# Optimization experiments

Measured on AMD Instinct MI355X. Metric: run time of the kernel, lower is better.

## Reference

```python
import jax, jax.numpy as jnp
import numpy as np

DISCOUNT = 0.99
HORIZON = 16


def setup_inputs() -> dict:
    key = jax.random.key(0)
    k1, k2, k3 = jax.random.split(key, 3)
    T, B = 1024, 4096
    rewards = jax.random.normal(k1, (T, B), dtype=jnp.float32)
    values = jax.random.normal(k2, (T, B), dtype=jnp.float32)
    masks = jax.random.uniform(k3, (T, B), dtype=jnp.float32)
    return {"rewards": rewards, "values": values, "masks": masks}


def _n_step_return(rewards, values, masks, gamma, horizon):
    # rewards/values/masks: [T, B]; time_axis == 0
    T = rewards.shape[0]
    rm = rewards * masks  # masked rewards
    # Pad end of time axis with zeros so every window has length `horizon`;
    # out-of-range rewards contribute 0, matching the truncated MC sum.
    pad = jnp.zeros((horizon - 1,) + rm.shape[1:], rm.dtype)
    rm_p = jnp.concatenate([rm, pad], axis=0)  # [T + horizon - 1, B]
    t = jnp.arange(T)
    idx = t[:, None] + jnp.arange(horizon)[None, :]  # [T, horizon]
    windows = rm_p[idx]  # [T, horizon, B]
    disc = jnp.asarray(gamma, rm.dtype) ** jnp.arange(horizon, dtype=rm.dtype)
    g = jnp.einsum('thb,h->tb', windows, disc)  # windowed discounted sums
    # Bootstrap: gamma^{effective_horizon} * V(s_{min(t+horizon-1, T-1)})
    eff_h = (jnp.minimum(t + horizon, T) - t).astype(rm.dtype)  # [T]
    v_idx = jnp.minimum(t + horizon - 1, T - 1)  # [T]
    g = g + (jnp.asarray(gamma, rm.dtype) ** eff_h)[:, None] * values[v_idx]
    return g


def reference(rewards, values, masks):
    return _n_step_return(rewards, values, masks, DISCOUNT, HORIZON)
```

## Files before the change

### kernel.cpp

```cpp
#include <hip/hip_runtime.h>


constexpr int   T_DIM  = 1024;
constexpr int   B_DIM  = 4096;
constexpr int   H      = 16;
constexpr int   CT     = 16;
constexpr int   HALO   = H - 1;
constexpr int   ROWS   = CT + HALO;
constexpr float GAMMA  = 0.99f;

constexpr float gpow_c(int n) {
    float g = 1.0f;
    for (int i = 0; i < n; ++i) g *= GAMMA;
    return g;
}
constexpr float G16 = gpow_c(16);

__global__ __launch_bounds__(256)
void NStepReturn_88691074662796_kernel(const float* __restrict__ rewards,
                                       const float* __restrict__ values,
                                       const float* __restrict__ masks,
                                       float* __restrict__ out)
{
    const int b  = blockIdx.x * 256 + threadIdx.x;
    const int t0 = blockIdx.y * CT;

    float r[ROWS], m[ROWS], v[CT];
    #pragma unroll
    for (int i = 0; i < ROWS; ++i) {
        const int t = t0 + i;
        if (t < T_DIM) {
            r[i] = rewards[t * B_DIM + b];
            m[i] = masks[t * B_DIM + b];
        } else {
            r[i] = 0.0f;
            m[i] = 0.0f;
        }
    }
    #pragma unroll
    for (int i = 0; i < CT; ++i) {
        const int vi = min(t0 + i + H - 1, T_DIM - 1);
        v[i] = values[vi * B_DIM + b];
    }

    #pragma unroll
    for (int i = 0; i < ROWS; ++i) r[i] *= m[i];

    float W = 0.0f;
    #pragma unroll
    for (int h = H - 1; h >= 0; --h) W = r[CT - 1 + h] + GAMMA * W;

    {
        const int t = t0 + CT - 1;
        float gb = G16;
        if (t + H > T_DIM) {
            gb = 1.0f;
            for (int k = 0; k < T_DIM - t; ++k) gb *= GAMMA;
        }
        out[t * B_DIM + b] = W + gb * v[CT - 1];
    }

    #pragma unroll
    for (int j = CT - 2; j >= 0; --j) {
        const int t = t0 + j;
        W = r[j] + GAMMA * W - G16 * r[j + H];

        float gb = G16;
        if (t + H > T_DIM) {
            gb = 1.0f;
            for (int k = 0; k < T_DIM - t; ++k) gb *= GAMMA;
        }
        out[t * B_DIM + b] = W + gb * v[j];
    }
}

extern "C" void kernel_launch(void* const* d_in, const int* in_sizes, int n_in,
                              void* d_out, int out_size, void* d_ws, size_t ws_size,
                              hipStream_t stream) {
    const float* rewards = (const float*)d_in[0];
    const float* values  = (const float*)d_in[1];
    const float* masks   = (const float*)d_in[2];
    float* out = (float*)d_out;

    dim3 grid(B_DIM / 256, T_DIM / CT);
    dim3 block(256);
    NStepReturn_88691074662796_kernel<<<grid, block, 0, stream>>>(rewards, values, masks, out);
}
```

Before: 89.82 us.

## Vectorize n-step return kernel with float4 and shrink time chunk

Each thread now processes four batch columns with float4 loads and stores, which cuts the number of memory instructions. The time chunk shrinks from 16 to 8 rows, and a launch-bounds occupancy hint is added to limit register pressure from the wider per-thread state. The smaller chunk raises the halo re-read overhead (23 rows read per 8 output rows instead of 31 per 16), trading extra memory traffic for more blocks and vector access.

```diff
diff --git a/kernel.cpp b/kernel.cpp
--- a/kernel.cpp
+++ b/kernel.cpp
@@ -3,8 +3,9 @@
 
 constexpr int   T_DIM  = 1024;
 constexpr int   B_DIM  = 4096;
+constexpr int   B4     = B_DIM / 4;
 constexpr int   H      = 16;
-constexpr int   CT     = 16;
+constexpr int   CT     = 8;
 constexpr int   HALO   = H - 1;
 constexpr int   ROWS   = CT + HALO;
 constexpr float GAMMA  = 0.99f;
@@ -16,39 +17,44 @@
 }
 constexpr float G16 = gpow_c(16);
 
-__global__ __launch_bounds__(256)
-void NStepReturn_88691074662796_kernel(const float* __restrict__ rewards,
-                                       const float* __restrict__ values,
-                                       const float* __restrict__ masks,
-                                       float* __restrict__ out)
+__global__ __launch_bounds__(256, 2)
+void NStepReturn_88691074662796_kernel(const float4* __restrict__ rewards,
+                                       const float4* __restrict__ values,
+                                       const float4* __restrict__ masks,
+                                       float4* __restrict__ out)
 {
-    const int b  = blockIdx.x * 256 + threadIdx.x;
+    const int c  = blockIdx.x * 256 + threadIdx.x;
     const int t0 = blockIdx.y * CT;
 
-    float r[ROWS], m[ROWS], v[CT];
+    float4 v[CT];
+    #pragma unroll
+    for (int i = 0; i < CT; ++i) {
+        const int vi = min(t0 + i + H - 1, T_DIM - 1);
+        v[i] = values[vi * B4 + c];
+    }
+
+    float4 rm[ROWS];
     #pragma unroll
     for (int i = 0; i < ROWS; ++i) {
         const int t = t0 + i;
         if (t < T_DIM) {
-            r[i] = rewards[t * B_DIM + b];
-            m[i] = masks[t * B_DIM + b];
+            const float4 r = rewards[t * B4 + c];
+            const float4 m = masks[t * B4 + c];
+            rm[i] = make_float4(r.x * m.x, r.y * m.y, r.z * m.z, r.w * m.w);
         } else {
-            r[i] = 0.0f;
-            m[i] = 0.0f;
+            rm[i] = make_float4(0.f, 0.f, 0.f, 0.f);
         }
     }
+
+    float4 W = make_float4(0.f, 0.f, 0.f, 0.f);
     #pragma unroll
-    for (int i = 0; i < CT; ++i) {
-        const int vi = min(t0 + i + H - 1, T_DIM - 1);
-        v[i] = values[vi * B_DIM + b];
+    for (int h = H - 1; h >= 0; --h) {
+        const float4 x = rm[CT - 1 + h];
+        W.x = x.x + GAMMA * W.x;
+        W.y = x.y + GAMMA * W.y;
+        W.z = x.z + GAMMA * W.z;
+        W.w = x.w + GAMMA * W.w;
     }
-
-    #pragma unroll
-    for (int i = 0; i < ROWS; ++i) r[i] *= m[i];
-
-    float W = 0.0f;
-    #pragma unroll
-    for (int h = H - 1; h >= 0; --h) W = r[CT - 1 + h] + GAMMA * W;
 
     {
         const int t = t0 + CT - 1;
@@ -57,32 +63,41 @@
             gb = 1.0f;
             for (int k = 0; k < T_DIM - t; ++k) gb *= GAMMA;
         }
-        out[t * B_DIM + b] = W + gb * v[CT - 1];
+        const float4 vv = v[CT - 1];
+        out[t * B4 + c] = make_float4(W.x + gb * vv.x, W.y + gb * vv.y,
+                                      W.z + gb * vv.z, W.w + gb * vv.w);
     }
 
     #pragma unroll
     for (int j = CT - 2; j >= 0; --j) {
         const int t = t0 + j;
-        W = r[j] + GAMMA * W - G16 * r[j + H];
+        const float4 x  = rm[j];
+        const float4 x16 = rm[j + H];
+        W.x = x.x + GAMMA * W.x - G16 * x16.x;
+        W.y = x.y + GAMMA * W.y - G16 * x16.y;
+        W.z = x.z + GAMMA * W.z - G16 * x16.z;
+        W.w = x.w + GAMMA * W.w - G16 * x16.w;
 
         float gb = G16;
         if (t + H > T_DIM) {
             gb = 1.0f;
             for (int k = 0; k < T_DIM - t; ++k) gb *= GAMMA;
         }
-        out[t * B_DIM + b] = W + gb * v[j];
+        const float4 vv = v[j];
+        out[t * B4 + c] = make_float4(W.x + gb * vv.x, W.y + gb * vv.y,
+                                      W.z + gb * vv.z, W.w + gb * vv.w);
     }
 }
 
 extern "C" void kernel_launch(void* const* d_in, const int* in_sizes, int n_in,
                               void* d_out, int out_size, void* d_ws, size_t ws_size,
                               hipStream_t stream) {
-    const float* rewards = (const float*)d_in[0];
-    const float* values  = (const float*)d_in[1];
-    const float* masks   = (const float*)d_in[2];
-    float* out = (float*)d_out;
+    const float4* rewards = (const float4*)d_in[0];
+    const float4* values  = (const float4*)d_in[1];
+    const float4* masks   = (const float4*)d_in[2];
+    float4* out = (float4*)d_out;
 
-    dim3 grid(B_DIM / 256, T_DIM / CT);
+    dim3 grid(B4 / 256, T_DIM / CT);
     dim3 block(256);
     NStepReturn_88691074662796_kernel<<<grid, block, 0, stream>>>(rewards, values, masks, out);
 }
```

After: 96.17 us. 1.07x slower.

## Vectorize to float2 columns and shrink time tile to four rows

Applied to the files above, without the earlier changes.

Each thread now handles two adjacent batch columns with float2 loads and stores, and the time tile per block drops from 16 to 4 rows. Launch bounds add a minimum-occupancy hint. The smaller tile raises the halo overhead: each block reads 19 rows of rewards and masks to produce 4 outputs, versus 31 for 16 before. That roughly doubles the input read traffic in exchange for more blocks, fewer registers per thread and wider memory accesses.

```diff
diff --git a/kernel.cpp b/kernel.cpp
--- a/kernel.cpp
+++ b/kernel.cpp
@@ -3,10 +3,10 @@
 
 constexpr int   T_DIM  = 1024;
 constexpr int   B_DIM  = 4096;
+constexpr int   B2     = B_DIM / 2;
 constexpr int   H      = 16;
-constexpr int   CT     = 16;
-constexpr int   HALO   = H - 1;
-constexpr int   ROWS   = CT + HALO;
+constexpr int   CT     = 4;
+constexpr int   ROWS   = CT + H - 1;
 constexpr float GAMMA  = 0.99f;
 
 constexpr float gpow_c(int n) {
@@ -16,39 +16,42 @@
 }
 constexpr float G16 = gpow_c(16);
 
-__global__ __launch_bounds__(256)
-void NStepReturn_88691074662796_kernel(const float* __restrict__ rewards,
-                                       const float* __restrict__ values,
-                                       const float* __restrict__ masks,
-                                       float* __restrict__ out)
+__global__ __launch_bounds__(256, 6)
+void NStepReturn_88691074662796_kernel(const float2* __restrict__ rewards,
+                                       const float2* __restrict__ values,
+                                       const float2* __restrict__ masks,
+                                       float2* __restrict__ out)
 {
-    const int b  = blockIdx.x * 256 + threadIdx.x;
+    const int c  = blockIdx.x * 256 + threadIdx.x;
     const int t0 = blockIdx.y * CT;
 
-    float r[ROWS], m[ROWS], v[CT];
+    float2 v[CT];
+    #pragma unroll
+    for (int i = 0; i < CT; ++i) {
+        const int vi = min(t0 + i + H - 1, T_DIM - 1);
+        v[i] = values[vi * B2 + c];
+    }
+
+    float2 rm[ROWS];
     #pragma unroll
     for (int i = 0; i < ROWS; ++i) {
         const int t = t0 + i;
         if (t < T_DIM) {
-            r[i] = rewards[t * B_DIM + b];
-            m[i] = masks[t * B_DIM + b];
+            const float2 r = rewards[t * B2 + c];
+            const float2 m = masks[t * B2 + c];
+            rm[i] = make_float2(r.x * m.x, r.y * m.y);
         } else {
-            r[i] = 0.0f;
-            m[i] = 0.0f;
+            rm[i] = make_float2(0.f, 0.f);
         }
     }
+
+    float2 W = make_float2(0.f, 0.f);
     #pragma unroll
-    for (int i = 0; i < CT; ++i) {
-        const int vi = min(t0 + i + H - 1, T_DIM - 1);
-        v[i] = values[vi * B_DIM + b];
+    for (int h = H - 1; h >= 0; --h) {
+        const float2 x = rm[CT - 1 + h];
+        W.x = x.x + GAMMA * W.x;
+        W.y = x.y + GAMMA * W.y;
     }
-
-    #pragma unroll
-    for (int i = 0; i < ROWS; ++i) r[i] *= m[i];
-
-    float W = 0.0f;
-    #pragma unroll
-    for (int h = H - 1; h >= 0; --h) W = r[CT - 1 + h] + GAMMA * W;
 
     {
         const int t = t0 + CT - 1;
@@ -57,32 +60,35 @@
             gb = 1.0f;
             for (int k = 0; k < T_DIM - t; ++k) gb *= GAMMA;
         }
-        out[t * B_DIM + b] = W + gb * v[CT - 1];
+        out[t * B2 + c] = make_float2(W.x + gb * v[CT - 1].x,
+                                      W.y + gb * v[CT - 1].y);
     }
 
     #pragma unroll
     for (int j = CT - 2; j >= 0; --j) {
         const int t = t0 + j;
-        W = r[j] + GAMMA * W - G16 * r[j + H];
+        W.x = rm[j].x + GAMMA * W.x - G16 * rm[j + H].x;
+        W.y = rm[j].y + GAMMA * W.y - G16 * rm[j + H].y;
 
         float gb = G16;
         if (t + H > T_DIM) {
             gb = 1.0f;
             for (int k = 0; k < T_DIM - t; ++k) gb *= GAMMA;
         }
-        out[t * B_DIM + b] = W + gb * v[j];
+        out[t * B2 + c] = make_float2(W.x + gb * v[j].x,
+                                      W.y + gb * v[j].y);
     }
 }
 
 extern "C" void kernel_launch(void* const* d_in, const int* in_sizes, int n_in,
                               void* d_out, int out_size, void* d_ws, size_t ws_size,
                               hipStream_t stream) {
-    const float* rewards = (const float*)d_in[0];
-    const float* values  = (const float*)d_in[1];
-    const float* masks   = (const float*)d_in[2];
-    float* out = (float*)d_out;
+    const float2* rewards = (const float2*)d_in[0];
+    const float2* values  = (const float2*)d_in[1];
+    const float2* masks   = (const float2*)d_in[2];
+    float2* out = (float2*)d_out;
 
-    dim3 grid(B_DIM / 256, T_DIM / CT);
+    dim3 grid(B2 / 256, T_DIM / CT);
     dim3 block(256);
     NStepReturn_88691074662796_kernel<<<grid, block, 0, stream>>>(rewards, values, masks, out);
 }
```

After: 96.30 us. 1.07x slower.
